# Kernel optimization log

Hardware: AMD Instinct MI355X
Metric: run time of the kernel (lower is better)

Reference implementation:

```python
import jax, jax.numpy as jnp
import numpy as np

EMBED = 768; HEADS = 12; DH = 64; DEPTH = 6; MLP = 3072
PATCH = (4, 16, 16)
N_PATCH = 2048          # (32/4)*(256/16)*(256/16)
N_REAL = N_PATCH + 1    # + cls token
S_PAD = 4096            # padded to multiple of max segment length
SEGS = [128, 256, 512, 1024, 2048]
RATIOS = [1, 2, 4, 8, 16]
NEG = -1e9


def _ln(x, w, b, eps=1e-5):
    m = jnp.mean(x, -1, keepdims=True)
    v = jnp.mean((x - m) ** 2, -1, keepdims=True)
    return (x - m) / jnp.sqrt(v + eps) * w + b


def dilated_attn(x, wq, bq, wk, bk, wv, bv, wo, bo):
    """LongNet dilated attention: per (segment w, ratio r) branch, split the
    sequence into segments of length w, keep every r-th token with a per-head
    offset (h % r), run dense attention inside the sparse segment, then combine
    branches per position/head with softmax-denominator (lse) weights."""
    B, S, E = x.shape
    q = (x @ wq + bq).reshape(B, S, HEADS, DH)
    k = (x @ wk + bk).reshape(B, S, HEADS, DH)
    v = (x @ wv + bv).reshape(B, S, HEADS, DH)
    scale = 1.0 / np.sqrt(DH).astype(np.float32)
    harr = jnp.arange(HEADS)[:, None]
    outs, lses = [], []
    for w, r in zip(SEGS, RATIOS):
        ns, m = S // w, w // r
        idx = (jnp.arange(HEADS)[:, None] % r) + r * jnp.arange(m)[None, :]  # [H, m]

        def seg(t):
            t = t.reshape(B, ns, w, HEADS, DH).transpose(0, 1, 3, 2, 4)  # B,ns,H,w,D
            return jnp.take_along_axis(t, idx[None, None, :, :, None], axis=3)

        qs, ks, vs = seg(q), seg(k), seg(v)  # [B, ns, H, m, D]
        pos = (jnp.arange(ns) * w)[:, None, None] + idx[None]  # [ns, H, m]
        kmask = jnp.where(pos < N_REAL, 0.0, NEG)  # mask padded keys
        sc = jnp.einsum('bnhqd,bnhkd->bnhqk', qs, ks) * scale + kmask[None, :, :, None, :]
        lse = jax.nn.logsumexp(sc, axis=-1)  # [B, ns, H, m]
        o = jnp.einsum('bnhqk,bnhkd->bnhqd', jax.nn.softmax(sc, axis=-1), vs)
        of = jnp.zeros((B, ns, HEADS, w, DH), x.dtype).at[:, :, harr, idx, :].set(o)
        lf = jnp.full((B, ns, HEADS, w), NEG, x.dtype).at[:, :, harr, idx].set(lse)
        outs.append(of.transpose(0, 1, 3, 2, 4).reshape(B, S, HEADS, DH))
        lses.append(lf.transpose(0, 1, 3, 2).reshape(B, S, HEADS))
    O = jnp.stack(outs)   # [Br, B, S, H, D]
    L = jnp.stack(lses)   # [Br, B, S, H]
    wts = jnp.exp(L - jnp.max(L, 0))
    wts = wts / jnp.sum(wts, 0)
    out = jnp.sum(O * wts[..., None], 0).reshape(B, S, E)
    return out @ wo + bo


def setup_inputs() -> dict:
    key = jax.random.key(0)
    ks = jax.random.split(key, 16)
    f = lambda k, shape: (0.02 * jax.random.normal(k, shape)).astype(jnp.float32)
    z = lambda *s: jnp.zeros(s, jnp.float32)
    o = lambda *s: jnp.ones(s, jnp.float32)
    return {
        'x': jax.random.normal(ks[0], (1, 1, 32, 256, 256), dtype=jnp.float32),
        'conv_w': f(ks[1], (EMBED, 1) + PATCH),
        'conv_b': z(EMBED),
        'cls_token': f(ks[2], (1, 1, EMBED)),
        'pos_embed': f(ks[3], (1, N_REAL, EMBED)),
        'ln1_w': o(DEPTH, EMBED), 'ln1_b': z(DEPTH, EMBED),
        'wq': f(ks[4], (DEPTH, EMBED, EMBED)), 'bq': z(DEPTH, EMBED),
        'wk': f(ks[5], (DEPTH, EMBED, EMBED)), 'bk': z(DEPTH, EMBED),
        'wv': f(ks[6], (DEPTH, EMBED, EMBED)), 'bv': z(DEPTH, EMBED),
        'wo': f(ks[7], (DEPTH, EMBED, EMBED)), 'bo': z(DEPTH, EMBED),
        'ln2_w': o(DEPTH, EMBED), 'ln2_b': z(DEPTH, EMBED),
        'w1': f(ks[8], (DEPTH, EMBED, MLP)), 'b1': z(DEPTH, MLP),
        'w2': f(ks[9], (DEPTH, MLP, EMBED)), 'b2': z(DEPTH, EMBED),
        'lnf_w': o(EMBED), 'lnf_b': z(EMBED),
    }


def reference(x, conv_w, conv_b, cls_token, pos_embed, ln1_w, ln1_b,
              wq, bq, wk, bk, wv, bv, wo, bo, ln2_w, ln2_b,
              w1, b1, w2, b2, lnf_w, lnf_b):
    # 3D patch embed: Conv3d stride=kernel=patch, then flatten spatial -> tokens
    p = jax.lax.conv_general_dilated(
        x, conv_w, window_strides=PATCH, padding='VALID',
        dimension_numbers=('NCDHW', 'OIDHW', 'NCDHW'))
    p = p + conv_b[None, :, None, None, None]
    B = p.shape[0]
    tok = p.reshape(B, EMBED, -1).transpose(0, 2, 1)  # [B, N_PATCH, E]
    tok = tok + pos_embed[:, 1:, :]
    cls = cls_token + pos_embed[:, :1, :]
    h = jnp.concatenate([jnp.broadcast_to(cls, (B, 1, EMBED)), tok], axis=1)
    h = jnp.pad(h, ((0, 0), (0, S_PAD - N_REAL), (0, 0)))  # pad to segment multiple

    params = {'ln1_w': ln1_w, 'ln1_b': ln1_b, 'wq': wq, 'bq': bq, 'wk': wk,
              'bk': bk, 'wv': wv, 'bv': bv, 'wo': wo, 'bo': bo,
              'ln2_w': ln2_w, 'ln2_b': ln2_b, 'w1': w1, 'b1': b1,
              'w2': w2, 'b2': b2}

    def layer(h, pr):
        a = dilated_attn(_ln(h, pr['ln1_w'], pr['ln1_b']),
                         pr['wq'], pr['bq'], pr['wk'], pr['bk'],
                         pr['wv'], pr['bv'], pr['wo'], pr['bo'])
        h = h + a
        f = _ln(h, pr['ln2_w'], pr['ln2_b'])
        f = jax.nn.gelu(f @ pr['w1'] + pr['b1'], approximate=False) @ pr['w2'] + pr['b2']
        return h + f, None

    h, _ = jax.lax.scan(layer, h, params)
    return _ln(h[:, 0], lnf_w, lnf_b)  # [B, EMBED]
```

## Files before the change

### kernel.cpp

```cpp
#include <hip/hip_runtime.h>
#include <math.h>

#define EMBED 768
#define HEADS 12
#define DH 64
#define DEPTH 6
#define MLP_DIM 3072
#define N_REAL 2049
#define SP 2112
#define SPAD 2176
#define NEGV (-1e9f)

typedef __attribute__((ext_vector_type(8))) short short8;
typedef __attribute__((ext_vector_type(4))) float f32x4;

__device__ __forceinline__ unsigned short f2bf(float f) {
    union { float f; unsigned u; } x; x.f = f;
    unsigned r = x.u + 0x7FFF + ((x.u >> 16) & 1);
    return (unsigned short)(r >> 16);
}
__device__ __forceinline__ float bf2f(unsigned short s) {
    union { unsigned u; float f; } x; x.u = (unsigned)s << 16;
    return x.f;
}

__device__ __forceinline__ size_t pidx(int mj, int k, int nkt) {
    return (((size_t)(mj >> 4) * nkt + (k >> 5)) << 9) + (size_t)((((k >> 3) & 3) * 16 + (mj & 15)) * 8 + (k & 7));
}

__global__ void im2col_kernel(const float* __restrict__ x, unsigned short* __restrict__ p) {
    const int pi = blockIdx.x;
    const int d = pi >> 8, rr = (pi >> 4) & 15, cc = pi & 15;
    const int t = threadIdx.x;
    #pragma unroll
    for (int u = 0; u < 4; ++u) {
        int i = u * 256 + t;
        int kd = i >> 8, kr = (i >> 4) & 15, kc = i & 15;
        float v = x[(size_t)(d * 4 + kd) * 65536 + (rr * 16 + kr) * 256 + (cc * 16 + kc)];
        p[pidx(pi, i, 32)] = f2bf(v);
    }
}

__device__ __forceinline__ void pack_KN_body(const float* __restrict__ src,
                                             unsigned short* __restrict__ dst,
                                             int N, int K, int bn, int bk) {
    __shared__ float lf[128][33];
    const int t = threadIdx.x;
    {
        const int kk = t >> 3, ch = t & 7;
        const float4* s = (const float4*)(src + (size_t)(bk * 32 + kk) * N + bn * 128 + ch * 16);
        float4 v0 = s[0], v1 = s[1], v2 = s[2], v3 = s[3];
        float tmp[16];
        ((float4*)tmp)[0] = v0; ((float4*)tmp)[1] = v1; ((float4*)tmp)[2] = v2; ((float4*)tmp)[3] = v3;
        #pragma unroll
        for (int u = 0; u < 16; ++u) lf[ch * 16 + u][kk] = tmp[u];
    }
    __syncthreads();
    const int nkt = K >> 5;
    const int cg = t >> 5;
    const int l0 = (t & 31) * 2;
    unsigned short* o = dst + (((size_t)(bn * 8 + cg) * nkt + bk) << 9);
    #pragma unroll
    for (int q = 0; q < 2; ++q) {
        const int l = l0 + q;
        const int col = cg * 16 + (l & 15), kb = (l >> 4) * 8;
        unsigned short ov[8];
        #pragma unroll
        for (int e = 0; e < 8; ++e) ov[e] = f2bf(lf[col][kb + e]);
        *(short8*)(o + l * 8) = *(short8*)ov;
    }
}

__global__ void pack_KN_kernel(const float* __restrict__ src, unsigned short* __restrict__ dst,
                               int N, int K) {
    pack_KN_body(src, dst, N, K, blockIdx.x, blockIdx.y);
}

__global__ void pack_KN4_kernel(const float* __restrict__ wq, const float* __restrict__ wk,
                                const float* __restrict__ wv, const float* __restrict__ wo,
                                unsigned short* __restrict__ qkv_pk, unsigned short* __restrict__ o_pk) {
    const int z = blockIdx.z;
    const float* src = (z == 0) ? wq : (z == 1) ? wk : (z == 2) ? wv : wo;
    unsigned short* dst = (z < 3) ? qkv_pk + (size_t)z * EMBED * EMBED : o_pk;
    pack_KN_body(src, dst, EMBED, EMBED, blockIdx.x, blockIdx.y);
}

__global__ void pack_NK_kernel(const float* __restrict__ src, unsigned short* __restrict__ dst,
                               int N, int K) {
    __shared__ float lf[128][33];
    const int bn = blockIdx.x, bk = blockIdx.y;
    const int t = threadIdx.x;
    {
        const int row = t >> 1, hf = t & 1;
        const float4* s = (const float4*)(src + (size_t)(bn * 128 + row) * K + bk * 32 + hf * 16);
        float4 v0 = s[0], v1 = s[1], v2 = s[2], v3 = s[3];
        float tmp[16];
        ((float4*)tmp)[0] = v0; ((float4*)tmp)[1] = v1; ((float4*)tmp)[2] = v2; ((float4*)tmp)[3] = v3;
        #pragma unroll
        for (int u = 0; u < 16; ++u) lf[row][hf * 16 + u] = tmp[u];
    }
    __syncthreads();
    const int nkt = K >> 5;
    const int cg = t >> 5;
    const int l0 = (t & 31) * 2;
    unsigned short* o = dst + (((size_t)(bn * 8 + cg) * nkt + bk) << 9);
    #pragma unroll
    for (int q = 0; q < 2; ++q) {
        const int l = l0 + q;
        const int col = cg * 16 + (l & 15), kb = (l >> 4) * 8;
        unsigned short ov[8];
        #pragma unroll
        for (int e = 0; e < 8; ++e) ov[e] = f2bf(lf[col][kb + e]);
        *(short8*)(o + l * 8) = *(short8*)ov;
    }
}

__global__ void concat_bias_kernel(const float* __restrict__ bq, const float* __restrict__ bk,
                                   const float* __restrict__ bv, float* __restrict__ bqkv) {
    int i = blockIdx.x * 256 + threadIdx.x;
    if (i >= DEPTH * 2304) return;
    int L = i / 2304, j = i - L * 2304;
    float v = (j < 768) ? bq[L * 768 + j] : (j < 1536) ? bk[L * 768 + j - 768] : bv[L * 768 + j - 1536];
    bqkv[i] = v;
}

__global__ void cls_init_kernel(const float* __restrict__ cls,
                                const float* __restrict__ pos,
                                float* __restrict__ h) {
    int e = blockIdx.x * 256 + threadIdx.x;
    if (e < EMBED) h[e] = cls[e] + pos[e];
}

template<bool PACKED>
__global__ void ln_kernel(const float* __restrict__ in, void* __restrict__ outv,
                          const float* __restrict__ w, const float* __restrict__ b,
                          int M) {
    int row = blockIdx.x;
    if (row >= M) return;
    const float* xr = in + (size_t)row * EMBED;
    int tid = threadIdx.x;
    float v0 = xr[tid], v1 = xr[tid + 256], v2 = xr[tid + 512];
    __shared__ float red[4];
    float s = v0 + v1 + v2;
    #pragma unroll
    for (int o = 32; o > 0; o >>= 1) s += __shfl_down(s, o);
    if ((tid & 63) == 0) red[tid >> 6] = s;
    __syncthreads();
    float mean = (red[0] + red[1] + red[2] + red[3]) * (1.0f / 768.0f);
    __syncthreads();
    float d0 = v0 - mean, d1 = v1 - mean, d2 = v2 - mean;
    float q2 = d0 * d0 + d1 * d1 + d2 * d2;
    #pragma unroll
    for (int o = 32; o > 0; o >>= 1) q2 += __shfl_down(q2, o);
    if ((tid & 63) == 0) red[tid >> 6] = q2;
    __syncthreads();
    float var = (red[0] + red[1] + red[2] + red[3]) * (1.0f / 768.0f);
    float rstd = 1.0f / sqrtf(var + 1e-5f);
    float o0 = d0 * rstd * w[tid]       + b[tid];
    float o1 = d1 * rstd * w[tid + 256] + b[tid + 256];
    float o2 = d2 * rstd * w[tid + 512] + b[tid + 512];
    if (PACKED) {
        unsigned short* o = (unsigned short*)outv;
        o[pidx(row, tid,       24)] = f2bf(o0);
        o[pidx(row, tid + 256, 24)] = f2bf(o1);
        o[pidx(row, tid + 512, 24)] = f2bf(o2);
    } else {
        float* orow = (float*)outv + (size_t)row * EMBED;
        orow[tid] = o0; orow[tid + 256] = o1; orow[tid + 512] = o2;
    }
}

template<int ACT, int MODE>
__global__ __launch_bounds__(256) __attribute__((amdgpu_waves_per_eu(2, 2)))
void gemm_bf16(const unsigned short* __restrict__ Apk, const unsigned short* __restrict__ Bpk,
               const float* __restrict__ bias, void* __restrict__ Cv,
               int M, int N, int K) {
    const int tid = threadIdx.x;
    const int lane = tid & 63;
    const int w4 = tid >> 6;
    const int wm = w4 >> 1, wn = w4 & 1;
    const int row0 = blockIdx.y * 128 + wm * 64, col0 = blockIdx.x * 128 + wn * 64;
    const int nktT = K >> 5;
    const int nk = nktT / gridDim.z;
    const int t0 = blockIdx.z * nk;

    f32x4 acc[4][4];
    #pragma unroll
    for (int mi = 0; mi < 4; ++mi)
        #pragma unroll
        for (int ni = 0; ni < 4; ++ni)
            #pragma unroll
            for (int j = 0; j < 4; ++j) acc[mi][ni][j] = 0.0f;

    const unsigned short* Ab[4];
    const unsigned short* Bb[4];
    #pragma unroll
    for (int i = 0; i < 4; ++i) {
        Ab[i] = Apk + (((size_t)(blockIdx.y * 8 + wm * 4 + i) * nktT + t0) << 9) + lane * 8;
        Bb[i] = Bpk + (((size_t)(blockIdx.x * 8 + wn * 4 + i) * nktT + t0) << 9) + lane * 8;
    }

    auto LOADT = [&](int t, short8* aa, short8* bb) {
        #pragma unroll
        for (int i = 0; i < 4; ++i) {
            aa[i] = *(const short8*)(Ab[i] + (size_t)t * 512);
            bb[i] = *(const short8*)(Bb[i] + (size_t)t * 512);
        }
    };
    auto MF = [&](short8* aa, short8* bb) {
        #pragma unroll
        for (int mi = 0; mi < 4; ++mi)
            #pragma unroll
            for (int ni = 0; ni < 4; ++ni)
                acc[mi][ni] = __builtin_amdgcn_mfma_f32_16x16x32_bf16(aa[mi], bb[ni], acc[mi][ni], 0, 0, 0);
    };

    short8 A0[4], B0[4], A1[4], B1[4], A2[4], B2[4], A3[4], B3[4];
    LOADT(0, A0, B0);
    LOADT(1, A1, B1);
    LOADT(2, A2, B2);
    for (int t = 0; t < nk; t += 4) {
        LOADT(t + 3, A3, B3);
        MF(A0, B0);
        if (t + 4 < nk) LOADT(t + 4, A0, B0);
        MF(A1, B1);
        if (t + 5 < nk) LOADT(t + 5, A1, B1);
        MF(A2, B2);
        if (t + 6 < nk) LOADT(t + 6, A2, B2);
        MF(A3, B3);
    }

    float* Cf = (float*)Cv;
    unsigned short* Cb = (unsigned short*)Cv;
    const int ln15 = lane & 15, kq = lane >> 4;
    const int nktN = N >> 5;
    const bool addb = (blockIdx.z == 0);
    #pragma unroll
    for (int mi = 0; mi < 4; ++mi) {
        #pragma unroll
        for (int ni = 0; ni < 4; ++ni) {
            const int col = col0 + ni * 16 + ln15;
            const float bb = addb ? bias[col] : 0.0f;
            #pragma unroll
            for (int j = 0; j < 4; ++j) {
                const int row = row0 + mi * 16 + kq * 4 + j;
                if (row < M) {
                    float v = acc[mi][ni][j] + bb;
                    if (ACT == 1) v = 0.5f * v * (1.0f + erff(v * 0.70710678118654752f));
                    if (MODE == 1)      atomicAdd(&Cf[(size_t)row * N + col], v);
                    else if (MODE == 2) Cb[(size_t)row * N + col] = f2bf(v);
                    else                Cb[pidx(row, col, nktN)] = f2bf(v);
                }
            }
        }
    }
}

__global__ __launch_bounds__(256, 1)
void attn_kernel(const unsigned short* __restrict__ qkv,
                 unsigned short* __restrict__ Obr, float* __restrict__ Lbr) {
    const int bx = blockIdx.x, hh = blockIdx.y;
    int b, n;
    if      (bx < 17) { b = 0; n = bx; }
    else if (bx < 26) { b = 1; n = bx - 17; }
    else if (bx < 31) { b = 2; n = bx - 26; }
    else if (bx < 34) { b = 3; n = bx - 31; }
    else              { b = 4; n = bx - 34; }
    const int r = 1 << b;
    const int segw = 128 << b;
    const int base = n * segw + (hh & (r - 1));

    __shared__ __attribute__((aligned(16))) unsigned short VT[64 * 128];
    __shared__ __attribute__((aligned(16))) unsigned short Pl[128 * 128];

    const int tid = threadIdx.x;

    {
        const int key = tid >> 1, dh2 = (tid & 1) * 32;
        const int pos = base + r * key;
        const bool val = pos < N_REAL;
        const unsigned short* vsrc = qkv + (size_t)(val ? pos : 0) * 2304 + 1536 + hh * 64 + dh2;
        #pragma unroll
        for (int u = 0; u < 4; ++u) {
            short8 vv = ((const short8*)vsrc)[u];
            #pragma unroll
            for (int e = 0; e < 8; ++e) {
                const int d = dh2 + u * 8 + e;
                VT[(d * 256 + ((key * 2) ^ ((d & 7) << 4))) >> 1] =
                    val ? (unsigned short)vv[e] : (unsigned short)0;
            }
        }
    }
    __syncthreads();

    const int lane = tid & 63, wv = tid >> 6;
    const int ln15 = lane & 15, kq = lane >> 4;

    f32x4 sc[2][8];
    #pragma unroll
    for (int mi = 0; mi < 2; ++mi)
        #pragma unroll
        for (int ni = 0; ni < 8; ++ni)
            #pragma unroll
            for (int j = 0; j < 4; ++j) sc[mi][ni][j] = 0.0f;

    #pragma unroll
    for (int kt = 0; kt < 2; ++kt) {
        short8 qfr[2], kfr[8];
        #pragma unroll
        for (int mi = 0; mi < 2; ++mi) {
            const int pos = base + r * (wv * 32 + mi * 16 + ln15);
            qfr[mi] = *(const short8*)(qkv + (size_t)(pos < N_REAL ? pos : 0) * 2304
                                       + hh * 64 + kt * 32 + kq * 8);
        }
        #pragma unroll
        for (int ni = 0; ni < 8; ++ni) {
            const int pos = base + r * (ni * 16 + ln15);
            kfr[ni] = *(const short8*)(qkv + (size_t)(pos < N_REAL ? pos : 0) * 2304
                                       + 768 + hh * 64 + kt * 32 + kq * 8);
        }
        #pragma unroll
        for (int mi = 0; mi < 2; ++mi)
            #pragma unroll
            for (int ni = 0; ni < 8; ++ni)
                sc[mi][ni] = __builtin_amdgcn_mfma_f32_16x16x32_bf16(qfr[mi], kfr[ni], sc[mi][ni], 0, 0, 0);
    }

    #pragma unroll
    for (int ni = 0; ni < 8; ++ni) {
        const bool kval = (base + r * (ni * 16 + ln15)) < N_REAL;
        #pragma unroll
        for (int mi = 0; mi < 2; ++mi)
            #pragma unroll
            for (int j = 0; j < 4; ++j)
                sc[mi][ni][j] = kval ? sc[mi][ni][j] * 0.125f : NEGV;
    }

    float rsum[2][4];
    #pragma unroll
    for (int mi = 0; mi < 2; ++mi) {
        #pragma unroll
        for (int j = 0; j < 4; ++j) {
            float mx = sc[mi][0][j];
            #pragma unroll
            for (int ni = 1; ni < 8; ++ni) mx = fmaxf(mx, sc[mi][ni][j]);
            mx = fmaxf(mx, __shfl_xor(mx, 1));
            mx = fmaxf(mx, __shfl_xor(mx, 2));
            mx = fmaxf(mx, __shfl_xor(mx, 4));
            mx = fmaxf(mx, __shfl_xor(mx, 8));
            float sm = 0.f;
            #pragma unroll
            for (int ni = 0; ni < 8; ++ni) {
                float e = __expf(sc[mi][ni][j] - mx);
                sc[mi][ni][j] = e;
                sm += e;
            }
            sm += __shfl_xor(sm, 1);
            sm += __shfl_xor(sm, 2);
            sm += __shfl_xor(sm, 4);
            sm += __shfl_xor(sm, 8);
            rsum[mi][j] = sm;
            const int prow = wv * 32 + mi * 16 + kq * 4 + j;
            const int qpos = base + r * prow;
            if (ln15 == 0 && qpos < N_REAL)
                Lbr[((size_t)b * SP + qpos) * HEADS + hh] = mx + logf(sm);
        }
    }

    #pragma unroll
    for (int mi = 0; mi < 2; ++mi)
        #pragma unroll
        for (int j = 0; j < 4; ++j) {
            const int prow = wv * 32 + mi * 16 + kq * 4 + j;
            #pragma unroll
            for (int ni = 0; ni < 8; ++ni) {
                const int col = ni * 16 + ln15;
                Pl[(prow * 256 + ((col * 2) ^ ((prow & 7) << 4))) >> 1] = f2bf(sc[mi][ni][j]);
            }
        }
    __syncthreads();

    f32x4 ov[2][4];
    #pragma unroll
    for (int mi = 0; mi < 2; ++mi)
        #pragma unroll
        for (int ni = 0; ni < 4; ++ni)
            #pragma unroll
            for (int j = 0; j < 4; ++j) ov[mi][ni][j] = 0.0f;

    #pragma unroll
    for (int kt = 0; kt < 4; ++kt) {
        short8 pa[2], vb[4];
        #pragma unroll
        for (int mi = 0; mi < 2; ++mi) {
            const int row = wv * 32 + mi * 16 + ln15;
            pa[mi] = *(const short8*)((const char*)Pl + row * 256
                                      + ((kt * 64 + kq * 16) ^ ((row & 7) << 4)));
        }
        #pragma unroll
        for (int ni = 0; ni < 4; ++ni) {
            const int d = ni * 16 + ln15;
            vb[ni] = *(const short8*)((const char*)VT + d * 256
                                      + ((kt * 64 + kq * 16) ^ ((d & 7) << 4)));
        }
        #pragma unroll
        for (int mi = 0; mi < 2; ++mi)
            #pragma unroll
            for (int ni = 0; ni < 4; ++ni)
                ov[mi][ni] = __builtin_amdgcn_mfma_f32_16x16x32_bf16(pa[mi], vb[ni], ov[mi][ni], 0, 0, 0);
    }

    #pragma unroll
    for (int mi = 0; mi < 2; ++mi)
        #pragma unroll
        for (int j = 0; j < 4; ++j) {
            const int prow = wv * 32 + mi * 16 + kq * 4 + j;
            const int qpos = base + r * prow;
            if (qpos < N_REAL) {
                const float inv = 1.0f / rsum[mi][j];
                #pragma unroll
                for (int ni = 0; ni < 4; ++ni)
                    Obr[((size_t)b * N_REAL + qpos) * EMBED + hh * 64 + ni * 16 + ln15] =
                        f2bf(ov[mi][ni][j] * inv);
            }
        }
}

__global__ void combine_kernel(const unsigned short* __restrict__ Obr, const float* __restrict__ Lbr,
                               unsigned short* __restrict__ out) {
    int gid = blockIdx.x * 256 + threadIdx.x;
    if (gid >= N_REAL * EMBED) return;
    int p = gid / EMBED, e = gid - p * EMBED;
    int h = e >> 6;
    float l[5];
    float mx = NEGV;
    #pragma unroll
    for (int b = 0; b < 5; ++b) {
        const int rm = (1 << b) - 1;
        l[b] = ((p & rm) == (h & rm)) ? Lbr[((size_t)b * SP + p) * HEADS + h] : NEGV;
        mx = fmaxf(mx, l[b]);
    }
    float wsum = 0.f, acc = 0.f;
    #pragma unroll
    for (int b = 0; b < 5; ++b) {
        if (l[b] > NEGV * 0.5f) {
            float wt = expf(l[b] - mx);
            wsum += wt;
            acc += wt * bf2f(Obr[((size_t)b * N_REAL + p) * EMBED + e]);
        }
    }
    out[pidx(p, e, 24)] = f2bf(acc / wsum);
}

extern "C" void kernel_launch(void* const* d_in, const int* in_sizes, int n_in,
                              void* d_out, int out_size, void* d_ws, size_t ws_size,
                              hipStream_t stream) {
    const float* x      = (const float*)d_in[0];
    const float* conv_w = (const float*)d_in[1];
    const float* conv_b = (const float*)d_in[2];
    const float* cls    = (const float*)d_in[3];
    const float* pos    = (const float*)d_in[4];
    const float* ln1w   = (const float*)d_in[5];
    const float* ln1b   = (const float*)d_in[6];
    const float* wq     = (const float*)d_in[7];
    const float* bq     = (const float*)d_in[8];
    const float* wk     = (const float*)d_in[9];
    const float* bk     = (const float*)d_in[10];
    const float* wv     = (const float*)d_in[11];
    const float* bv     = (const float*)d_in[12];
    const float* wo     = (const float*)d_in[13];
    const float* bo     = (const float*)d_in[14];
    const float* ln2w   = (const float*)d_in[15];
    const float* ln2b   = (const float*)d_in[16];
    const float* w1     = (const float*)d_in[17];
    const float* b1     = (const float*)d_in[18];
    const float* w2     = (const float*)d_in[19];
    const float* b2     = (const float*)d_in[20];
    const float* lnfw   = (const float*)d_in[21];
    const float* lnfb   = (const float*)d_in[22];

    float* ws = (float*)d_ws;
    float* h     = ws;  ws += (size_t)SP * EMBED;
    float* Lbr   = ws;  ws += (size_t)5 * SP * HEADS;
    float* bqkv  = ws;  ws += (size_t)DEPTH * 2304;
    unsigned short* qkv_bf   = (unsigned short*)ws;  ws += (size_t)SPAD * 2304 / 2;
    unsigned short* xln_pk   = (unsigned short*)ws;  ws += (size_t)SPAD * EMBED / 2;
    unsigned short* attn_pk  = (unsigned short*)ws;  ws += (size_t)SPAD * EMBED / 2;
    unsigned short* mid_pk   = (unsigned short*)ws;  ws += (size_t)SPAD * MLP_DIM / 2;
    unsigned short* patch_pk = (unsigned short*)ws;  ws += (size_t)2112 * 1024 / 2;
    unsigned short* convw_pk = (unsigned short*)ws;  ws += (size_t)EMBED * 1024 / 2;
    unsigned short* Obr      = (unsigned short*)ws;  ws += (size_t)5 * N_REAL * EMBED / 2 + 64;
    unsigned short* wqkv_pk  = (unsigned short*)ws;  ws += (size_t)2304 * EMBED / 2;
    unsigned short* wo_pk    = (unsigned short*)ws;  ws += (size_t)EMBED * EMBED / 2;
    unsigned short* w1_pk    = (unsigned short*)ws;  ws += (size_t)MLP_DIM * EMBED / 2;
    unsigned short* w2_pk    = (unsigned short*)ws;  ws += (size_t)EMBED * MLP_DIM / 2;

    im2col_kernel<<<2048, 256, 0, stream>>>(x, patch_pk);
    pack_NK_kernel<<<dim3(6, 32), 256, 0, stream>>>(conv_w, convw_pk, EMBED, 1024);
    concat_bias_kernel<<<(DEPTH * 2304 + 255) / 256, 256, 0, stream>>>(bq, bk, bv, bqkv);
    cls_init_kernel<<<3, 256, 0, stream>>>(cls, pos, h);
    hipMemcpyAsync(h + EMBED, pos + EMBED, (size_t)2048 * EMBED * sizeof(float),
                   hipMemcpyDeviceToDevice, stream);
    gemm_bf16<0, 1><<<dim3(6, 16, 2), 256, 0, stream>>>(patch_pk, convw_pk, conv_b,
                                                        h + EMBED, 2048, EMBED, 1024);

    for (int L = 0; L < DEPTH; ++L) {
        const size_t EE = (size_t)EMBED * EMBED;
        const size_t EM = (size_t)EMBED * MLP_DIM;
        pack_KN4_kernel<<<dim3(6, 24, 4), 256, 0, stream>>>(wq + L * EE, wk + L * EE,
                                                            wv + L * EE, wo + L * EE,
                                                            wqkv_pk, wo_pk);
        pack_KN_kernel<<<dim3(24, 24), 256, 0, stream>>>(w1 + L * EM, w1_pk, MLP_DIM, EMBED);
        pack_KN_kernel<<<dim3(6, 96),  256, 0, stream>>>(w2 + L * EM, w2_pk, EMBED, MLP_DIM);

        ln_kernel<true><<<N_REAL, 256, 0, stream>>>(h, xln_pk, ln1w + (size_t)L * EMBED,
                                                    ln1b + (size_t)L * EMBED, N_REAL);
        gemm_bf16<0, 2><<<dim3(18, 17), 256, 0, stream>>>(xln_pk, wqkv_pk, bqkv + (size_t)L * 2304,
                                                          qkv_bf, N_REAL, 2304, EMBED);
        attn_kernel<<<dim3(36, 12), 256, 0, stream>>>(qkv_bf, Obr, Lbr);
        combine_kernel<<<((N_REAL * EMBED) + 255) / 256, 256, 0, stream>>>(Obr, Lbr, attn_pk);
        gemm_bf16<0, 1><<<dim3(6, 17, 2), 256, 0, stream>>>(attn_pk, wo_pk, bo + (size_t)L * EMBED,
                                                            h, N_REAL, EMBED, EMBED);
        ln_kernel<true><<<N_REAL, 256, 0, stream>>>(h, xln_pk, ln2w + (size_t)L * EMBED,
                                                    ln2b + (size_t)L * EMBED, N_REAL);
        gemm_bf16<1, 3><<<dim3(24, 17), 256, 0, stream>>>(xln_pk, w1_pk, b1 + (size_t)L * MLP_DIM,
                                                          mid_pk, N_REAL, MLP_DIM, EMBED);
        gemm_bf16<0, 1><<<dim3(6, 17, 2), 256, 0, stream>>>(mid_pk, w2_pk, b2 + (size_t)L * EMBED,
                                                            h, N_REAL, EMBED, MLP_DIM);
    }

    ln_kernel<false><<<1, 256, 0, stream>>>(h, (float*)d_out, lnfw, lnfb, 1);
}
```

Baseline: 1.084 ms.

## Remap GEMM workgroups XCD-contiguously, shorten prefetch pipeline, merge weight-pack launches

The GEMM now takes a flattened 1D grid and remaps block ids so that each XCD (id & 7) handles a contiguous range of output tiles, aiming for better L2 reuse of A/B panels on the chiplet design. The register prefetch depth drops from 4 stages to 2, and the waves_per_eu(2,2) attribute is removed, which trades some latency hiding for fewer registers and possibly higher occupancy. The three per-layer weight-pack launches are merged into one kernel to cut launch overhead. The shallower pipeline could expose more global-load latency.

```diff
diff --git a/kernel.cpp b/kernel.cpp
--- a/kernel.cpp
+++ b/kernel.cpp
@@ -71,18 +71,24 @@
     }
 }
 
-__global__ void pack_KN_kernel(const float* __restrict__ src, unsigned short* __restrict__ dst,
-                               int N, int K) {
-    pack_KN_body(src, dst, N, K, blockIdx.x, blockIdx.y);
-}
-
-__global__ void pack_KN4_kernel(const float* __restrict__ wq, const float* __restrict__ wk,
+__global__ void pack_all_kernel(const float* __restrict__ wq, const float* __restrict__ wk,
                                 const float* __restrict__ wv, const float* __restrict__ wo,
-                                unsigned short* __restrict__ qkv_pk, unsigned short* __restrict__ o_pk) {
-    const int z = blockIdx.z;
-    const float* src = (z == 0) ? wq : (z == 1) ? wk : (z == 2) ? wv : wo;
-    unsigned short* dst = (z < 3) ? qkv_pk + (size_t)z * EMBED * EMBED : o_pk;
-    pack_KN_body(src, dst, EMBED, EMBED, blockIdx.x, blockIdx.y);
+                                const float* __restrict__ w1s, const float* __restrict__ w2s,
+                                unsigned short* __restrict__ qkv_pk, unsigned short* __restrict__ o_pk,
+                                unsigned short* __restrict__ w1_pk, unsigned short* __restrict__ w2_pk) {
+    const int fid = blockIdx.x;
+    if (fid < 576) {
+        const int m = fid / 144, r = fid % 144;
+        const float* src = (m == 0) ? wq : (m == 1) ? wk : (m == 2) ? wv : wo;
+        unsigned short* dst = (m < 3) ? qkv_pk + (size_t)m * EMBED * EMBED : o_pk;
+        pack_KN_body(src, dst, EMBED, EMBED, r % 6, r / 6);
+    } else if (fid < 1152) {
+        const int r = fid - 576;
+        pack_KN_body(w1s, w1_pk, MLP_DIM, EMBED, r % 24, r / 24);
+    } else {
+        const int r = fid - 1152;
+        pack_KN_body(w2s, w2_pk, EMBED, MLP_DIM, r % 6, r / 6);
+    }
 }
 
 __global__ void pack_NK_kernel(const float* __restrict__ src, unsigned short* __restrict__ dst,
@@ -171,18 +177,28 @@
 }
 
 template<int ACT, int MODE>
-__global__ __launch_bounds__(256) __attribute__((amdgpu_waves_per_eu(2, 2)))
+__global__ __launch_bounds__(256)
 void gemm_bf16(const unsigned short* __restrict__ Apk, const unsigned short* __restrict__ Bpk,
                const float* __restrict__ bias, void* __restrict__ Cv,
-               int M, int N, int K) {
+               int M, int N, int K, int nx, int ny, int nz) {
+    const int nwg = nx * ny * nz;
+    const int fid = blockIdx.x;
+    const int xcd = fid & 7, slot = fid >> 3;
+    const int qq = nwg >> 3, rr2 = nwg & 7;
+    const int orig = (xcd < rr2 ? xcd * (qq + 1) : rr2 * (qq + 1) + (xcd - rr2) * qq) + slot;
+    const int bx = orig % nx;
+    const int tzy = orig / nx;
+    const int bz = tzy % nz;
+    const int by = tzy / nz;
+
     const int tid = threadIdx.x;
     const int lane = tid & 63;
     const int w4 = tid >> 6;
     const int wm = w4 >> 1, wn = w4 & 1;
-    const int row0 = blockIdx.y * 128 + wm * 64, col0 = blockIdx.x * 128 + wn * 64;
+    const int row0 = by * 128 + wm * 64, col0 = bx * 128 + wn * 64;
     const int nktT = K >> 5;
-    const int nk = nktT / gridDim.z;
-    const int t0 = blockIdx.z * nk;
+    const int nk = nktT / nz;
+    const int t0 = bz * nk;
 
     f32x4 acc[4][4];
     #pragma unroll
@@ -196,8 +212,8 @@
     const unsigned short* Bb[4];
     #pragma unroll
     for (int i = 0; i < 4; ++i) {
-        Ab[i] = Apk + (((size_t)(blockIdx.y * 8 + wm * 4 + i) * nktT + t0) << 9) + lane * 8;
-        Bb[i] = Bpk + (((size_t)(blockIdx.x * 8 + wn * 4 + i) * nktT + t0) << 9) + lane * 8;
+        Ab[i] = Apk + (((size_t)(by * 8 + wm * 4 + i) * nktT + t0) << 9) + lane * 8;
+        Bb[i] = Bpk + (((size_t)(bx * 8 + wn * 4 + i) * nktT + t0) << 9) + lane * 8;
     }
 
     auto LOADT = [&](int t, short8* aa, short8* bb) {
@@ -215,26 +231,20 @@
                 acc[mi][ni] = __builtin_amdgcn_mfma_f32_16x16x32_bf16(aa[mi], bb[ni], acc[mi][ni], 0, 0, 0);
     };
 
-    short8 A0[4], B0[4], A1[4], B1[4], A2[4], B2[4], A3[4], B3[4];
+    short8 A0[4], B0[4], A1[4], B1[4];
     LOADT(0, A0, B0);
-    LOADT(1, A1, B1);
-    LOADT(2, A2, B2);
-    for (int t = 0; t < nk; t += 4) {
-        LOADT(t + 3, A3, B3);
+    for (int t = 0; t < nk; t += 2) {
+        LOADT(t + 1, A1, B1);
         MF(A0, B0);
-        if (t + 4 < nk) LOADT(t + 4, A0, B0);
+        if (t + 2 < nk) LOADT(t + 2, A0, B0);
         MF(A1, B1);
-        if (t + 5 < nk) LOADT(t + 5, A1, B1);
-        MF(A2, B2);
-        if (t + 6 < nk) LOADT(t + 6, A2, B2);
-        MF(A3, B3);
     }
 
     float* Cf = (float*)Cv;
     unsigned short* Cb = (unsigned short*)Cv;
     const int ln15 = lane & 15, kq = lane >> 4;
     const int nktN = N >> 5;
-    const bool addb = (blockIdx.z == 0);
+    const bool addb = (bz == 0);
     #pragma unroll
     for (int mi = 0; mi < 4; ++mi) {
         #pragma unroll
@@ -501,32 +511,30 @@
     cls_init_kernel<<<3, 256, 0, stream>>>(cls, pos, h);
     hipMemcpyAsync(h + EMBED, pos + EMBED, (size_t)2048 * EMBED * sizeof(float),
                    hipMemcpyDeviceToDevice, stream);
-    gemm_bf16<0, 1><<<dim3(6, 16, 2), 256, 0, stream>>>(patch_pk, convw_pk, conv_b,
-                                                        h + EMBED, 2048, EMBED, 1024);
+    gemm_bf16<0, 1><<<192, 256, 0, stream>>>(patch_pk, convw_pk, conv_b,
+                                             h + EMBED, 2048, EMBED, 1024, 6, 16, 2);
 
     for (int L = 0; L < DEPTH; ++L) {
         const size_t EE = (size_t)EMBED * EMBED;
         const size_t EM = (size_t)EMBED * MLP_DIM;
-        pack_KN4_kernel<<<dim3(6, 24, 4), 256, 0, stream>>>(wq + L * EE, wk + L * EE,
-                                                            wv + L * EE, wo + L * EE,
-                                                            wqkv_pk, wo_pk);
-        pack_KN_kernel<<<dim3(24, 24), 256, 0, stream>>>(w1 + L * EM, w1_pk, MLP_DIM, EMBED);
-        pack_KN_kernel<<<dim3(6, 96),  256, 0, stream>>>(w2 + L * EM, w2_pk, EMBED, MLP_DIM);
+        pack_all_kernel<<<1728, 256, 0, stream>>>(wq + L * EE, wk + L * EE, wv + L * EE,
+                                                  wo + L * EE, w1 + L * EM, w2 + L * EM,
+                                                  wqkv_pk, wo_pk, w1_pk, w2_pk);
 
         ln_kernel<true><<<N_REAL, 256, 0, stream>>>(h, xln_pk, ln1w + (size_t)L * EMBED,
                                                     ln1b + (size_t)L * EMBED, N_REAL);
-        gemm_bf16<0, 2><<<dim3(18, 17), 256, 0, stream>>>(xln_pk, wqkv_pk, bqkv + (size_t)L * 2304,
-                                                          qkv_bf, N_REAL, 2304, EMBED);
+        gemm_bf16<0, 2><<<306, 256, 0, stream>>>(xln_pk, wqkv_pk, bqkv + (size_t)L * 2304,
+                                                 qkv_bf, N_REAL, 2304, EMBED, 18, 17, 1);
         attn_kernel<<<dim3(36, 12), 256, 0, stream>>>(qkv_bf, Obr, Lbr);
         combine_kernel<<<((N_REAL * EMBED) + 255) / 256, 256, 0, stream>>>(Obr, Lbr, attn_pk);
-        gemm_bf16<0, 1><<<dim3(6, 17, 2), 256, 0, stream>>>(attn_pk, wo_pk, bo + (size_t)L * EMBED,
-                                                            h, N_REAL, EMBED, EMBED);
+        gemm_bf16<0, 1><<<204, 256, 0, stream>>>(attn_pk, wo_pk, bo + (size_t)L * EMBED,
+                                                 h, N_REAL, EMBED, EMBED, 6, 17, 2);
         ln_kernel<true><<<N_REAL, 256, 0, stream>>>(h, xln_pk, ln2w + (size_t)L * EMBED,
                                                     ln2b + (size_t)L * EMBED, N_REAL);
-        gemm_bf16<1, 3><<<dim3(24, 17), 256, 0, stream>>>(xln_pk, w1_pk, b1 + (size_t)L * MLP_DIM,
-                                                          mid_pk, N_REAL, MLP_DIM, EMBED);
-        gemm_bf16<0, 1><<<dim3(6, 17, 2), 256, 0, stream>>>(mid_pk, w2_pk, b2 + (size_t)L * EMBED,
-                                                            h, N_REAL, EMBED, MLP_DIM);
+        gemm_bf16<1, 3><<<408, 256, 0, stream>>>(xln_pk, w1_pk, b1 + (size_t)L * MLP_DIM,
+                                                 mid_pk, N_REAL, MLP_DIM, EMBED, 24, 17, 1);
+        gemm_bf16<0, 1><<<204, 256, 0, stream>>>(mid_pk, w2_pk, b2 + (size_t)L * EMBED,
+                                                 h, N_REAL, EMBED, MLP_DIM, 6, 17, 2);
     }
 
     ln_kernel<false><<<1, 256, 0, stream>>>(h, (float*)d_out, lnfw, lnfb, 1);
```

Result: no change. 1.083 ms (-0.1%).
